# Optimization experiments

Measured on AMD Instinct MI355X. Metric: run time of the kernel, lower is better.

Reference implementation:

```python
import jax, jax.numpy as jnp
import numpy as np


def setup_inputs() -> dict:
    key = jax.random.key(0)
    k0, k1, k2, k3 = jax.random.split(key, 4)
    B, I, S = 4, 16, 4096      # batch, inDim, nSeq
    O, W = 64, 64
    T = 32768                  # nRealLen (output timeline length)
    x = jax.random.normal(k0, (B, I, S), dtype=jnp.float32)
    bound = float(np.sqrt(1.0 / (I * W)))  # torch uniform init of LTITRFGen
    weight = jax.random.uniform(k1, (O, I, W), dtype=jnp.float32, minval=-bound, maxval=bound)
    bias = jax.random.uniform(k2, (O,), dtype=jnp.float32, minval=-bound, maxval=bound)
    # strictly increasing, unique event onset indices per batch (scatter-set == scatter-add)
    stride = (T - W) // S  # = 7
    jitter = jax.random.randint(k3, (B, S), 0, stride)
    sourceIdx = (jnp.arange(S, dtype=jnp.int32)[None, :] * stride + jitter.astype(jnp.int32))
    return {"x": x, "weight": weight, "bias": bias, "sourceIdx": sourceIdx, "nRealLen": T}


def reference(x, weight, bias, sourceIdx, nRealLen):
    # x: (B, inDim, nSeq); weight: (outDim, inDim, nWin); bias: (outDim,)
    # sourceIdx: (B, nSeq) int, unique & sorted per batch; nRealLen: python int
    B, I, S = x.shape
    O, _, W = weight.shape
    # LTITRFGen (ifAddBiasInForward=False): sum over inDim of outer product
    trfs = jnp.einsum('bis,oiw->bows', x, weight)  # (B, O, W, S)
    # TRFAligner: scatter each TRF at its onset, then overlap-add (F.fold).
    # out[b, o, src[b,s] + w] += trfs[b, o, w, s]; trim to nRealLen.
    Tpad = nRealLen + W - 1
    tidx = sourceIdx[:, None, :] + jnp.arange(W, dtype=sourceIdx.dtype)[:, None]  # (B, W, S)

    def scatter_one(trf_b, tidx_b):
        # trf_b: (O, W, S), tidx_b: (W, S)
        return jnp.zeros((O, Tpad), dtype=trf_b.dtype).at[:, tidx_b.reshape(-1)].add(
            trf_b.reshape(O, -1))

    out = jax.vmap(scatter_one)(trfs, tidx)  # (B, O, Tpad)
    # ASTRF.forward adds the LTI bias per output channel
    return out[:, :, :nRealLen] + bias[:, None]
```

## Files before the change

kernel.cpp:

```cpp
#include <hip/hip_runtime.h>


#define BB 4
#define II 16
#define SS 4096
#define OO 64
#define WW 64
#define TLEN 32768
#define KK 1024
#define KC 128
#define TT 256
#define YROWPAD 24
#define AROWPAD 136
#define YR 32848

typedef short bf16x8 __attribute__((ext_vector_type(8)));
typedef float f32x4  __attribute__((ext_vector_type(4)));

static __device__ __forceinline__ ushort f2bf(float f) {
    union { float f; uint u; } v; v.f = f;
    const uint u = v.u;
    return (ushort)((u + 0x7FFFu + ((u >> 16) & 1u)) >> 16);
}

__global__ void prep_w(const float* __restrict__ w, ushort* __restrict__ w2) {
    const int idx = blockIdx.x * 256 + threadIdx.x;
    const int o = idx >> 10, i = (idx >> 6) & 15, d = idx & 63;
    w2[o * KK + d * II + i] = f2bf(w[idx]);
}

__global__ void scat_y(const float* __restrict__ x, const int* __restrict__ srcIdx,
                       ushort* __restrict__ y) {
    __shared__ float tile[II][64 + 1];
    const int b = blockIdx.y, e0 = blockIdx.x * 64, tid = threadIdx.x;
    const int i = tid >> 6, el = tid & 63;
    #pragma unroll
    for (int k = 0; k < 4; ++k)
        tile[i + 4 * k][el] = x[((size_t)(b * II + i + 4 * k)) * SS + e0 + el];
    __syncthreads();
    const int e = tid >> 2, iq = tid & 3;
    ushort4 v;
    v.x = f2bf(tile[4 * iq + 0][e]);
    v.y = f2bf(tile[4 * iq + 1][e]);
    v.z = f2bf(tile[4 * iq + 2][e]);
    v.w = f2bf(tile[4 * iq + 3][e]);
    const int row = 64 + srcIdx[b * SS + e0 + e];
    *(ushort4*)(y + ((size_t)b * YR + row) * II + iq * 4) = v;
}

__global__ __launch_bounds__(256, 2) void astrf_mfma(
    const ushort* __restrict__ w2,
    const ushort* __restrict__ y,
    const float* __restrict__ bias,
    float* __restrict__ out)
{
    __shared__ __align__(16) ushort yt[320 * YROWPAD];
    __shared__ __align__(16) ushort aL[2][OO * AROWPAD];
    __shared__ float sbias[OO];

    const int tid  = threadIdx.x;
    const int t0   = blockIdx.x * TT;
    const int b    = blockIdx.y;
    const int wave = tid >> 6, lane = tid & 63;
    const int nl   = lane & 15, kg = lane >> 4;

    {
        const uint4* src = (const uint4*)(y + ((size_t)b * YR + (t0 + 1)) * II);
        for (int c = tid; c < 640; c += 256) {
            const int p = c >> 1, h = c & 1;
            const uint4 v = src[p * 2 + h];
            *(uint4*)&yt[p * YROWPAD + h * 8] = v;
        }
    }
    if (tid < OO) sbias[tid] = bias[tid];

    uint4 pf[4];
    #pragma unroll
    for (int j = 0; j < 4; ++j) {
        const int u = tid + j * 256, o = u >> 4, q = u & 15;
        pf[j] = *(const uint4*)(w2 + (size_t)o * KK + q * 8);
    }
    #pragma unroll
    for (int j = 0; j < 4; ++j) {
        const int u = tid + j * 256, o = u >> 4, q = u & 15;
        *(uint4*)&aL[0][o * AROWPAD + q * 8] = pf[j];
    }
    __syncthreads();

    f32x4 acc[4][4];
    #pragma unroll
    for (int m = 0; m < 4; ++m)
        #pragma unroll
        for (int n = 0; n < 4; ++n)
            acc[m][n] = (f32x4){0.f, 0.f, 0.f, 0.f};

    for (int kc = 0; kc < 8; ++kc) {
        if (kc < 7) {
            #pragma unroll
            for (int j = 0; j < 4; ++j) {
                const int u = tid + j * 256, o = u >> 4, q = u & 15;
                pf[j] = *(const uint4*)(w2 + (size_t)o * KK + (kc + 1) * KC + q * 8);
            }
        }
        const ushort* aB = aL[kc & 1];
        #pragma unroll
        for (int ks = 0; ks < 4; ++ks) {
            bf16x8 afr[4];
            const int koff = ks * 32 + kg * 8;
            #pragma unroll
            for (int m = 0; m < 4; ++m)
                afr[m] = *(const bf16x8*)&aB[(m * 16 + nl) * AROWPAD + koff];
            const int d  = kc * 8 + ks * 2 + (kg >> 1);
            const int i0 = (kg & 1) * 8;
            #pragma unroll
            for (int n = 0; n < 4; ++n) {
                const int p = (wave * 4 + n) * 16 + nl + 63 - d;
                const bf16x8 bfr = *(const bf16x8*)&yt[p * YROWPAD + i0];
                #pragma unroll
                for (int m = 0; m < 4; ++m)
                    acc[m][n] = __builtin_amdgcn_mfma_f32_16x16x32_bf16(
                        afr[m], bfr, acc[m][n], 0, 0, 0);
            }
        }
        if (kc < 7) {
            #pragma unroll
            for (int j = 0; j < 4; ++j) {
                const int u = tid + j * 256, o = u >> 4, q = u & 15;
                *(uint4*)&aL[(kc + 1) & 1][o * AROWPAD + q * 8] = pf[j];
            }
        }
        __syncthreads();
    }

    #pragma unroll
    for (int m = 0; m < 4; ++m)
        #pragma unroll
        for (int n = 0; n < 4; ++n) {
            const int t = t0 + (wave * 4 + n) * 16 + nl;
            #pragma unroll
            for (int r = 0; r < 4; ++r) {
                const int o = m * 16 + kg * 4 + r;
                out[((size_t)(b * OO + o)) * TLEN + t] = acc[m][n][r] + sbias[o];
            }
        }
}

extern "C" void kernel_launch(void* const* d_in, const int* in_sizes, int n_in,
                              void* d_out, int out_size, void* d_ws, size_t ws_size,
                              hipStream_t stream) {
    const float* x    = (const float*)d_in[0];
    const float* wgt  = (const float*)d_in[1];
    const float* bias = (const float*)d_in[2];
    const int*   src  = (const int*)d_in[3];
    float* out = (float*)d_out;

    ushort* w2 = (ushort*)d_ws;
    ushort* y  = (ushort*)((char*)d_ws + 131072);

    prep_w<<<dim3(OO * KK / 256), 256, 0, stream>>>(wgt, w2);
    hipMemsetAsync(y, 0, (size_t)BB * YR * II * sizeof(ushort), stream);
    scat_y<<<dim3(SS / 64, BB), 256, 0, stream>>>(x, src, y);
    astrf_mfma<<<dim3(TLEN / TT, BB), 256, 0, stream>>>(w2, y, bias, out);
}
```

Before: 92.42 us.

## Fuse prep kernels, scatter events into LDS per tile, stream weights from global

```diff
diff --git a/kernel.cpp b/kernel.cpp
--- a/kernel.cpp
+++ b/kernel.cpp
@@ -1,18 +1,16 @@
 #include <hip/hip_runtime.h>
 
 
-#define BB 4
-#define II 16
-#define SS 4096
-#define OO 64
-#define WW 64
+#define BB   4
+#define II   16
+#define SS   4096
+#define OO   64
+#define WW   64
 #define TLEN 32768
-#define KK 1024
-#define KC 128
-#define TT 256
-#define YROWPAD 24
-#define AROWPAD 136
-#define YR 32848
+#define KK   1024
+#define TT   256
+#define YROWS 320
+#define YPAD  24
 
 typedef short bf16x8 __attribute__((ext_vector_type(8)));
 typedef float f32x4  __attribute__((ext_vector_type(4)));
@@ -23,16 +21,17 @@
     return (ushort)((u + 0x7FFFu + ((u >> 16) & 1u)) >> 16);
 }
 
-__global__ void prep_w(const float* __restrict__ w, ushort* __restrict__ w2) {
-    const int idx = blockIdx.x * 256 + threadIdx.x;
-    const int o = idx >> 10, i = (idx >> 6) & 15, d = idx & 63;
-    w2[o * KK + d * II + i] = f2bf(w[idx]);
-}
-
-__global__ void scat_y(const float* __restrict__ x, const int* __restrict__ srcIdx,
-                       ushort* __restrict__ y) {
+__global__ void prep(const float* __restrict__ x, const float* __restrict__ w,
+                     ushort* __restrict__ w2, ushort* __restrict__ xtb) {
+    const int bid = blockIdx.x, tid = threadIdx.x;
+    if (bid < 256) {
+        const int idx = bid * 256 + tid;
+        const int o = idx >> 10, i = (idx >> 6) & 15, d = idx & 63;
+        w2[o * KK + d * II + i] = f2bf(w[idx]);
+        return;
+    }
     __shared__ float tile[II][64 + 1];
-    const int b = blockIdx.y, e0 = blockIdx.x * 64, tid = threadIdx.x;
+    const int b = (bid - 256) >> 6, e0 = ((bid - 256) & 63) * 64;
     const int i = tid >> 6, el = tid & 63;
     #pragma unroll
     for (int k = 0; k < 4; ++k)
@@ -44,19 +43,17 @@
     v.y = f2bf(tile[4 * iq + 1][e]);
     v.z = f2bf(tile[4 * iq + 2][e]);
     v.w = f2bf(tile[4 * iq + 3][e]);
-    const int row = 64 + srcIdx[b * SS + e0 + e];
-    *(ushort4*)(y + ((size_t)b * YR + row) * II + iq * 4) = v;
+    *(ushort4*)(xtb + ((size_t)(b * SS + e0 + e)) * II + iq * 4) = v;
 }
 
-__global__ __launch_bounds__(256, 2) void astrf_mfma(
+__global__ __launch_bounds__(256, 3) void astrf_mfma(
     const ushort* __restrict__ w2,
-    const ushort* __restrict__ y,
+    const ushort* __restrict__ xtb,
+    const int*   __restrict__ srcIdx,
     const float* __restrict__ bias,
     float* __restrict__ out)
 {
-    __shared__ __align__(16) ushort yt[320 * YROWPAD];
-    __shared__ __align__(16) ushort aL[2][OO * AROWPAD];
-    __shared__ float sbias[OO];
+    __shared__ __align__(16) ushort yt[YROWS * YPAD];
 
     const int tid  = threadIdx.x;
     const int t0   = blockIdx.x * TT;
@@ -64,85 +61,87 @@
     const int wave = tid >> 6, lane = tid & 63;
     const int nl   = lane & 15, kg = lane >> 4;
 
+    uint4* z4 = (uint4*)yt;
+    for (int c = tid; c < YROWS * YPAD / 8; c += 256)
+        z4[c] = (uint4){0u, 0u, 0u, 0u};
+
+    const int* sp = srcIdx + b * SS;
+    const int tmin = t0 - (WW - 1);
+    const int tmax = t0 + TT;
+    int e_lo = tmin > 6 ? (tmin - 6) / 7 : 0;  if (e_lo > SS) e_lo = SS;
+    while (e_lo > 0 && sp[e_lo - 1] >= tmin) --e_lo;
+    while (e_lo < SS && sp[e_lo] < tmin) ++e_lo;
+    int e_hi = tmax > 0 ? tmax / 7 : 0;  if (e_hi > SS) e_hi = SS;
+    while (e_hi > 0 && sp[e_hi - 1] >= tmax) --e_hi;
+    while (e_hi < SS && sp[e_hi] < tmax) ++e_hi;
+    __syncthreads();
+
     {
-        const uint4* src = (const uint4*)(y + ((size_t)b * YR + (t0 + 1)) * II);
-        for (int c = tid; c < 640; c += 256) {
-            const int p = c >> 1, h = c & 1;
-            const uint4 v = src[p * 2 + h];
-            *(uint4*)&yt[p * YROWPAD + h * 8] = v;
+        const int idx = tid >> 2, part = tid & 3;
+        if (idx < e_hi - e_lo) {
+            const int e = e_lo + idx;
+            const int p = sp[e] - t0 + 63;
+            const uint2 v = *(const uint2*)(xtb + ((size_t)(b * SS + e)) * II + part * 4);
+            *(uint2*)&yt[p * YPAD + part * 4] = v;
         }
     }
-    if (tid < OO) sbias[tid] = bias[tid];
 
-    uint4 pf[4];
+    float bv[4];
     #pragma unroll
-    for (int j = 0; j < 4; ++j) {
-        const int u = tid + j * 256, o = u >> 4, q = u & 15;
-        pf[j] = *(const uint4*)(w2 + (size_t)o * KK + q * 8);
-    }
+    for (int n = 0; n < 4; ++n) bv[n] = bias[n * 16 + nl];
+    const int abase = (wave * 64 + nl + 63 - (kg >> 1)) * YPAD + (kg & 1) * 8;
+    const ushort* wb[4];
     #pragma unroll
-    for (int j = 0; j < 4; ++j) {
-        const int u = tid + j * 256, o = u >> 4, q = u & 15;
-        *(uint4*)&aL[0][o * AROWPAD + q * 8] = pf[j];
-    }
+    for (int n = 0; n < 4; ++n) wb[n] = w2 + (size_t)(n * 16 + nl) * KK + kg * 8;
+
     __syncthreads();
 
     f32x4 acc[4][4];
     #pragma unroll
-    for (int m = 0; m < 4; ++m)
+    for (int mi = 0; mi < 4; ++mi)
         #pragma unroll
         for (int n = 0; n < 4; ++n)
-            acc[m][n] = (f32x4){0.f, 0.f, 0.f, 0.f};
+            acc[mi][n] = (f32x4){0.f, 0.f, 0.f, 0.f};
 
-    for (int kc = 0; kc < 8; ++kc) {
-        if (kc < 7) {
+    bf16x8 A[2][4], Bf[2][4];
+    #pragma unroll
+    for (int mi = 0; mi < 4; ++mi) A[0][mi] = *(const bf16x8*)&yt[abase + mi * 16 * YPAD];
+    #pragma unroll
+    for (int n = 0; n < 4; ++n)   Bf[0][n] = *(const bf16x8*)(wb[n]);
+
+    #pragma unroll
+    for (int ks = 0; ks < 32; ++ks) {
+        const int cu = ks & 1, nx = cu ^ 1;
+        if (ks < 31) {
             #pragma unroll
-            for (int j = 0; j < 4; ++j) {
-                const int u = tid + j * 256, o = u >> 4, q = u & 15;
-                pf[j] = *(const uint4*)(w2 + (size_t)o * KK + (kc + 1) * KC + q * 8);
-            }
+            for (int mi = 0; mi < 4; ++mi)
+                A[nx][mi] = *(const bf16x8*)&yt[abase - (ks + 1) * 2 * YPAD + mi * 16 * YPAD];
+            #pragma unroll
+            for (int n = 0; n < 4; ++n)
+                Bf[nx][n] = *(const bf16x8*)(wb[n] + (ks + 1) * 32);
         }
-        const ushort* aB = aL[kc & 1];
         #pragma unroll
-        for (int ks = 0; ks < 4; ++ks) {
-            bf16x8 afr[4];
-            const int koff = ks * 32 + kg * 8;
+        for (int n = 0; n < 4; ++n)
             #pragma unroll
-            for (int m = 0; m < 4; ++m)
-                afr[m] = *(const bf16x8*)&aB[(m * 16 + nl) * AROWPAD + koff];
-            const int d  = kc * 8 + ks * 2 + (kg >> 1);
-            const int i0 = (kg & 1) * 8;
-            #pragma unroll
-            for (int n = 0; n < 4; ++n) {
-                const int p = (wave * 4 + n) * 16 + nl + 63 - d;
-                const bf16x8 bfr = *(const bf16x8*)&yt[p * YROWPAD + i0];
-                #pragma unroll
-                for (int m = 0; m < 4; ++m)
-                    acc[m][n] = __builtin_amdgcn_mfma_f32_16x16x32_bf16(
-                        afr[m], bfr, acc[m][n], 0, 0, 0);
-            }
-        }
-        if (kc < 7) {
-            #pragma unroll
-            for (int j = 0; j < 4; ++j) {
-                const int u = tid + j * 256, o = u >> 4, q = u & 15;
-                *(uint4*)&aL[(kc + 1) & 1][o * AROWPAD + q * 8] = pf[j];
-            }
-        }
-        __syncthreads();
+            for (int mi = 0; mi < 4; ++mi)
+                acc[mi][n] = __builtin_amdgcn_mfma_f32_16x16x32_bf16(
+                    A[cu][mi], Bf[cu][n], acc[mi][n], 0, 0, 0);
     }
 
     #pragma unroll
-    for (int m = 0; m < 4; ++m)
+    for (int mi = 0; mi < 4; ++mi) {
+        const int t = t0 + wave * 64 + mi * 16 + kg * 4;
         #pragma unroll
         for (int n = 0; n < 4; ++n) {
-            const int t = t0 + (wave * 4 + n) * 16 + nl;
-            #pragma unroll
-            for (int r = 0; r < 4; ++r) {
-                const int o = m * 16 + kg * 4 + r;
-                out[((size_t)(b * OO + o)) * TLEN + t] = acc[m][n][r] + sbias[o];
-            }
+            const int o = n * 16 + nl;
+            float4 v;
+            v.x = acc[mi][n][0] + bv[n];
+            v.y = acc[mi][n][1] + bv[n];
+            v.z = acc[mi][n][2] + bv[n];
+            v.w = acc[mi][n][3] + bv[n];
+            *(float4*)(out + ((size_t)(b * OO + o)) * TLEN + t) = v;
         }
+    }
 }
 
 extern "C" void kernel_launch(void* const* d_in, const int* in_sizes, int n_in,
@@ -154,11 +153,9 @@
     const int*   src  = (const int*)d_in[3];
     float* out = (float*)d_out;
 
-    ushort* w2 = (ushort*)d_ws;
-    ushort* y  = (ushort*)((char*)d_ws + 131072);
+    ushort* w2  = (ushort*)d_ws;
+    ushort* xtb = (ushort*)((char*)d_ws + 131072);
 
-    prep_w<<<dim3(OO * KK / 256), 256, 0, stream>>>(wgt, w2);
-    hipMemsetAsync(y, 0, (size_t)BB * YR * II * sizeof(ushort), stream);
-    scat_y<<<dim3(SS / 64, BB), 256, 0, stream>>>(x, src, y);
-    astrf_mfma<<<dim3(TLEN / TT, BB), 256, 0, stream>>>(w2, y, bias, out);
+    prep<<<dim3(512), 256, 0, stream>>>(x, wgt, w2, xtb);
+    astrf_mfma<<<dim3(TLEN / TT, BB), 256, 0, stream>>>(w2, xtb, src, bias, out);
 }
```

Measured after the change: 111.2 us. 20.4% more time.
